# Performance work log

Hardware: AMD Instinct MI355X
Metric: run time of the kernel (lower is better)

The kernel has to match this reference:

```python
import jax, jax.numpy as jnp
import numpy as np

N, E, G = 50000, 800000, 64
IN_C, HID, HEADS, OUT_C = 128, 64, 4, 10
NEG_SLOPE = 0.2
EPS = 1e-16


def gat_conv(x, src, dst, W, a_src, a_dst, bias, heads, out_ch):
    # x: [N, F_in]; W: [F_in, heads*out_ch]; a_*: [heads, out_ch]; bias: [heads*out_ch]
    n = x.shape[0]
    h = (x @ W).reshape(n, heads, out_ch)                     # [N, H, C]
    alpha_src = jnp.einsum('nhc,hc->nh', h, a_src)            # [N, H]
    alpha_dst = jnp.einsum('nhc,hc->nh', h, a_dst)            # [N, H]
    e = jax.nn.leaky_relu(alpha_src[src] + alpha_dst[dst], NEG_SLOPE)  # [E, H]
    # segment softmax over incoming edges of each destination node
    m = jax.ops.segment_max(e, dst, num_segments=n)
    ex = jnp.exp(e - m[dst])
    denom = jax.ops.segment_sum(ex, dst, num_segments=n)
    alpha = ex / (denom[dst] + EPS)                           # [E, H]
    msg = h[src] * alpha[:, :, None]                          # [E, H, C]
    out = jax.ops.segment_sum(msg, dst, num_segments=n)       # [N, H, C]
    return out.reshape(n, heads * out_ch) + bias


def setup_inputs() -> dict:
    key = jax.random.key(0)
    ks = jax.random.split(key, 16)
    s = 0.1
    inp = {
        'x': jax.random.normal(ks[0], (N, IN_C), dtype=jnp.float32),
        'edge_index': jax.random.randint(ks[1], (2, E), 0, N, dtype=jnp.int64)
            if jax.config.jax_enable_x64 else jax.random.randint(ks[1], (2, E), 0, N).astype(jnp.int32),
        'batch': jnp.sort(jax.random.randint(ks[2], (N,), 0, G).astype(jnp.int32)),
        'W1': s * jax.random.normal(ks[3], (IN_C, HEADS * HID), dtype=jnp.float32),
        'as1': s * jax.random.normal(ks[4], (HEADS, HID), dtype=jnp.float32),
        'ad1': s * jax.random.normal(ks[5], (HEADS, HID), dtype=jnp.float32),
        'b1': jnp.zeros((HEADS * HID,), jnp.float32),
        'W2': s * jax.random.normal(ks[6], (HEADS * HID, HEADS * HID), dtype=jnp.float32),
        'as2': s * jax.random.normal(ks[7], (HEADS, HID), dtype=jnp.float32),
        'ad2': s * jax.random.normal(ks[8], (HEADS, HID), dtype=jnp.float32),
        'b2': jnp.zeros((HEADS * HID,), jnp.float32),
        'W3': s * jax.random.normal(ks[9], (HEADS * HID, HID), dtype=jnp.float32),
        'as3': s * jax.random.normal(ks[10], (1, HID), dtype=jnp.float32),
        'ad3': s * jax.random.normal(ks[11], (1, HID), dtype=jnp.float32),
        'b3': jnp.zeros((HID,), jnp.float32),
        'Wc': s * jax.random.normal(ks[12], (HID, OUT_C), dtype=jnp.float32),
        'bc': jnp.zeros((OUT_C,), jnp.float32),
    }
    return inp


def reference(x, edge_index, batch, W1, as1, ad1, b1, W2, as2, ad2, b2,
              W3, as3, ad3, b3, Wc, bc):
    n = x.shape[0]
    loop = jnp.arange(n, dtype=edge_index.dtype)
    src = jnp.concatenate([edge_index[0], loop])  # add self-loops (PyG default)
    dst = jnp.concatenate([edge_index[1], loop])

    h = gat_conv(x, src, dst, W1, as1, ad1, b1, HEADS, HID)
    h = jax.nn.elu(h)
    h = gat_conv(h, src, dst, W2, as2, ad2, b2, HEADS, HID)
    h = jax.nn.elu(h)
    h = gat_conv(h, src, dst, W3, as3, ad3, b3, 1, HID)

    # global mean pool over graphs
    sums = jax.ops.segment_sum(h, batch, num_segments=G)            # [G, HID]
    counts = jax.ops.segment_sum(jnp.ones((n,), h.dtype), batch, num_segments=G)
    pooled = sums / jnp.maximum(counts, 1.0)[:, None]

    logits = pooled @ Wc + bc                                       # [G, OUT_C]
    return logits
```

## Files before the change

### kernel.cpp

```cpp
#include <hip/hip_runtime.h>

#define NEG_SLOPE 0.2f
#define EPSV 1e-16f

typedef unsigned short ushort_t;
typedef __attribute__((ext_vector_type(8))) short bf16x8;
typedef __attribute__((ext_vector_type(4))) float f32x4;

__device__ __forceinline__ ushort_t f2bf(float f) {
    union { float f; unsigned u; } v; v.f = f;
    unsigned r = v.u + 0x7FFFu + ((v.u >> 16) & 1u);
    return (ushort_t)(r >> 16);
}
__device__ __forceinline__ float bf2f(ushort_t u) {
    union { unsigned u; float f; } v; v.u = ((unsigned)u) << 16;
    return v.f;
}

__global__ __launch_bounds__(256)
void count_kernel(const int* __restrict__ ei, int* __restrict__ deg, int E, int n) {
    int i = blockIdx.x * blockDim.x + threadIdx.x;
    int M = E + n;
    if (i >= M) return;
    int d = (i < E) ? ei[E + i] : (i - E);
    atomicAdd(&deg[d], 1);
}

__global__ __launch_bounds__(1024)
void scan1_kernel(const int* __restrict__ deg, int* __restrict__ indptr,
                  int* __restrict__ bsum, int n) {
    __shared__ int wsum[16];
    const int t = threadIdx.x;
    const int lane = t & 63;
    const int w = t >> 6;
    const int i = blockIdx.x * 1024 + t;
    int v = (i < n) ? deg[i] : 0;
    int s = v;
    #pragma unroll
    for (int off = 1; off < 64; off <<= 1) {
        int u = __shfl_up(s, off);
        if (lane >= off) s += u;
    }
    if (lane == 63) wsum[w] = s;
    __syncthreads();
    if (t < 16) {
        int ws_ = wsum[t];
        #pragma unroll
        for (int off = 1; off < 16; off <<= 1) {
            int u = __shfl_up(ws_, off);
            if (t >= off) ws_ += u;
        }
        wsum[t] = ws_;
    }
    __syncthreads();
    int woff = (w > 0) ? wsum[w - 1] : 0;
    if (i < n) indptr[i + 1] = woff + s;
    if (t == 0) bsum[blockIdx.x] = wsum[15];
}

__global__ __launch_bounds__(64)
void scan2_kernel(int* __restrict__ bsum, int nb) {
    int t = threadIdx.x;
    int v = (t < nb) ? bsum[t] : 0;
    int s = v;
    #pragma unroll
    for (int off = 1; off < 64; off <<= 1) {
        int u = __shfl_up(s, off);
        if (t >= off) s += u;
    }
    if (t < nb) bsum[t] = s - v;
}

__global__ __launch_bounds__(1024)
void scan3_kernel(int* __restrict__ indptr, const int* __restrict__ bsum, int n) {
    int i = blockIdx.x * 1024 + threadIdx.x;
    if (i < n) indptr[i + 1] += bsum[blockIdx.x];
    if (i == 0) indptr[0] = 0;
}

__global__ __launch_bounds__(256)
void scatter_kernel(const int* __restrict__ ei, int* __restrict__ cursor,
                    int* __restrict__ csr_src, int E, int n) {
    int i = blockIdx.x * blockDim.x + threadIdx.x;
    int M = E + n;
    if (i >= M) return;
    int s, d;
    if (i < E) { s = ei[i]; d = ei[E + i]; }
    else       { s = i - E; d = i - E; }
    int pos = atomicAdd(&cursor[d], 1);
    csr_src[pos] = s;
}

__global__ __launch_bounds__(256)
void cvt_kernel(const float* __restrict__ in, ushort_t* __restrict__ out, int n4) {
    int i = blockIdx.x * blockDim.x + threadIdx.x;
    if (i >= n4) return;
    float4 v = *reinterpret_cast<const float4*>(&in[i * 4]);
    ushort4 o;
    o.x = f2bf(v.x); o.y = f2bf(v.y); o.z = f2bf(v.z); o.w = f2bf(v.w);
    *reinterpret_cast<ushort4*>(&out[i * 4]) = o;
}

__global__ __launch_bounds__(256)
void transW_kernel(const float* __restrict__ W, ushort_t* __restrict__ Wt, int K, int N) {
    int idx = blockIdx.x * blockDim.x + threadIdx.x;
    if (idx >= K * N) return;
    int n = idx % N, k = idx / N;
    Wt[(long)n * K + k] = f2bf(W[idx]);
}

__global__ __launch_bounds__(256)
void mfma_gemm_alpha_kernel(const ushort_t* __restrict__ A, const ushort_t* __restrict__ Wt,
                            ushort_t* __restrict__ C,
                            const float* __restrict__ a_src, const float* __restrict__ a_dst,
                            float* __restrict__ asrc, float* __restrict__ adst,
                            int M, int K, int N, int H) {
    __shared__ ushort_t As[128][40];
    __shared__ ushort_t Ws[64][40];
    const int tid = threadIdx.x;
    const int w   = tid >> 6;
    const int lane = tid & 63;
    const int l15 = lane & 15;
    const int l4  = lane >> 4;
    const int row0 = blockIdx.x * 128;
    const int col0 = blockIdx.y * 64;
    const int hd   = blockIdx.y;

    f32x4 acc[2][4];
    #pragma unroll
    for (int mi = 0; mi < 2; ++mi)
        #pragma unroll
        for (int ni = 0; ni < 4; ++ni)
            acc[mi][ni] = (f32x4){0.f, 0.f, 0.f, 0.f};

    for (int k0 = 0; k0 < K; k0 += 32) {
        #pragma unroll
        for (int it = 0; it < 2; ++it) {
            int idx = tid + it * 256;
            int r = idx >> 2, seg = idx & 3;
            int gr = row0 + r;
            uint4 v = make_uint4(0u, 0u, 0u, 0u);
            if (gr < M)
                v = *reinterpret_cast<const uint4*>(&A[(long)gr * K + k0 + seg * 8]);
            *reinterpret_cast<uint4*>(&As[r][seg * 8]) = v;
        }
        {
            int r = tid >> 2, seg = tid & 3;
            uint4 v = *reinterpret_cast<const uint4*>(&Wt[(long)(col0 + r) * K + k0 + seg * 8]);
            *reinterpret_cast<uint4*>(&Ws[r][seg * 8]) = v;
        }
        __syncthreads();
        bf16x8 af[2], bfr[4];
        #pragma unroll
        for (int mi = 0; mi < 2; ++mi)
            af[mi] = *reinterpret_cast<const bf16x8*>(&As[w * 32 + mi * 16 + l15][8 * l4]);
        #pragma unroll
        for (int ni = 0; ni < 4; ++ni)
            bfr[ni] = *reinterpret_cast<const bf16x8*>(&Ws[ni * 16 + l15][8 * l4]);
        #pragma unroll
        for (int mi = 0; mi < 2; ++mi)
            #pragma unroll
            for (int ni = 0; ni < 4; ++ni)
                acc[mi][ni] = __builtin_amdgcn_mfma_f32_16x16x32_bf16(
                    af[mi], bfr[ni], acc[mi][ni], 0, 0, 0);
        __syncthreads();
    }

    #pragma unroll
    for (int mi = 0; mi < 2; ++mi)
        #pragma unroll
        for (int reg = 0; reg < 4; ++reg) {
            int gr = row0 + w * 32 + mi * 16 + l4 * 4 + reg;
            if (gr < M) {
                #pragma unroll
                for (int ni = 0; ni < 4; ++ni)
                    C[(long)gr * N + col0 + ni * 16 + l15] = f2bf(acc[mi][ni][reg]);
            }
        }

    float aS[4], aD[4];
    #pragma unroll
    for (int ni = 0; ni < 4; ++ni) {
        aS[ni] = a_src[hd * 64 + ni * 16 + l15];
        aD[ni] = a_dst[hd * 64 + ni * 16 + l15];
    }
    #pragma unroll
    for (int mi = 0; mi < 2; ++mi)
        #pragma unroll
        for (int reg = 0; reg < 4; ++reg) {
            float s = 0.f, d = 0.f;
            #pragma unroll
            for (int ni = 0; ni < 4; ++ni) {
                s += acc[mi][ni][reg] * aS[ni];
                d += acc[mi][ni][reg] * aD[ni];
            }
            #pragma unroll
            for (int off = 1; off < 16; off <<= 1) {
                s += __shfl_xor(s, off);
                d += __shfl_xor(d, off);
            }
            int gr = row0 + w * 32 + mi * 16 + l4 * 4 + reg;
            if (l15 == 0 && gr < M) {
                asrc[gr * H + hd] = s;
                adst[gr * H + hd] = d;
            }
        }
}

__global__ __launch_bounds__(256)
void aggregate4_kernel(const ushort_t* __restrict__ h, const float* __restrict__ asrc,
                       const float* __restrict__ adst, const int* __restrict__ indptr,
                       const int* __restrict__ csr_src, const float* __restrict__ bias,
                       ushort_t* __restrict__ out, int n, int apply_elu) {
    __shared__ int   sOff[4][64];
    __shared__ float sEx[4][4][68];
    const int node = (blockIdx.x * blockDim.x + threadIdx.x) >> 6;
    const int lane = threadIdx.x & 63;
    const int w    = threadIdx.x >> 6;
    if (node >= n) return;
    const int hd   = lane >> 4;
    const int eidx = lane & 15;
    const int beg = indptr[node], end = indptr[node + 1];
    const float ad = adst[node * 4 + hd];
    const ushort_t* __restrict__ hrow = h + 4 * lane;

    float m = -3.4e38f, sum_ex = 0.f;
    float ax = 0.f, ay = 0.f, az = 0.f, aw = 0.f;
    for (int cb = beg; cb < end; cb += 64) {
        const int cnt = min(64, end - cb);
        int s[4];
        float e[4];
        #pragma unroll
        for (int j = 0; j < 4; ++j) {
            int idx = eidx + 16 * j;
            s[j] = (idx < cnt) ? csr_src[cb + idx] : 0;
        }
        #pragma unroll
        for (int j = 0; j < 4; ++j) {
            float t = asrc[s[j] * 4 + hd] + ad;
            t = t > 0.f ? t : NEG_SLOPE * t;
            e[j] = (eidx + 16 * j < cnt) ? t : -3.4e38f;
        }
        float cm = fmaxf(fmaxf(e[0], e[1]), fmaxf(e[2], e[3]));
        #pragma unroll
        for (int off = 1; off < 16; off <<= 1) cm = fmaxf(cm, __shfl_xor(cm, off));
        const float nm = fmaxf(m, cm);
        const float scale = __expf(m - nm);
        float ex[4];
        #pragma unroll
        for (int j = 0; j < 4; ++j)
            ex[j] = (eidx + 16 * j < cnt) ? __expf(e[j] - nm) : 0.f;
        float csum = (ex[0] + ex[1]) + (ex[2] + ex[3]);
        #pragma unroll
        for (int off = 1; off < 16; off <<= 1) csum += __shfl_xor(csum, off);
        sum_ex = sum_ex * scale + csum;
        ax *= scale; ay *= scale; az *= scale; aw *= scale;
        m = nm;
        #pragma unroll
        for (int j = 0; j < 4; ++j) sEx[w][hd][eidx + 16 * j] = ex[j];
        if (hd == 0) {
            #pragma unroll
            for (int j = 0; j < 4; ++j) sOff[w][eidx + 16 * j] = s[j] << 8;
        }
        int i = 0;
        for (; i + 8 <= cnt; i += 8) {
            int o[8];
            float ee[8];
            ushort4 v[8];
            #pragma unroll
            for (int u = 0; u < 8; ++u) o[u] = sOff[w][i + u];
            #pragma unroll
            for (int u = 0; u < 8; ++u) v[u] = *reinterpret_cast<const ushort4*>(hrow + o[u]);
            #pragma unroll
            for (int u = 0; u < 8; ++u) ee[u] = sEx[w][hd][i + u];
            #pragma unroll
            for (int u = 0; u < 8; ++u) {
                ax += ee[u] * bf2f(v[u].x);
                ay += ee[u] * bf2f(v[u].y);
                az += ee[u] * bf2f(v[u].z);
                aw += ee[u] * bf2f(v[u].w);
            }
        }
        for (; i < cnt; ++i) {
            int o = sOff[w][i];
            float ee = sEx[w][hd][i];
            ushort4 v = *reinterpret_cast<const ushort4*>(hrow + o);
            ax += ee * bf2f(v.x); ay += ee * bf2f(v.y);
            az += ee * bf2f(v.z); aw += ee * bf2f(v.w);
        }
    }
    const float inv = 1.f / (sum_ex + EPSV);
    float4 b4 = *reinterpret_cast<const float4*>(bias + 4 * lane);
    float ox = ax * inv + b4.x;
    float oy = ay * inv + b4.y;
    float oz = az * inv + b4.z;
    float ow = aw * inv + b4.w;
    if (apply_elu) {
        ox = ox > 0.f ? ox : expm1f(ox);
        oy = oy > 0.f ? oy : expm1f(oy);
        oz = oz > 0.f ? oz : expm1f(oz);
        ow = ow > 0.f ? ow : expm1f(ow);
    }
    ushort4 o4;
    o4.x = f2bf(ox); o4.y = f2bf(oy); o4.z = f2bf(oz); o4.w = f2bf(ow);
    *reinterpret_cast<ushort4*>(out + (long)node * 256 + 4 * lane) = o4;
}

__global__ __launch_bounds__(256)
void aggregate_kernel(const ushort_t* __restrict__ h, const float* __restrict__ asrc,
                      const float* __restrict__ adst, const int* __restrict__ indptr,
                      const int* __restrict__ csr_src, const float* __restrict__ bias,
                      float* __restrict__ out, int n, int apply_elu) {
    __shared__ int   sInd[4][64];
    __shared__ float sEx[4][64];
    const int node = (blockIdx.x * blockDim.x + threadIdx.x) >> 6;
    const int lane = threadIdx.x & 63;
    const int w    = threadIdx.x >> 6;
    if (node >= n) return;
    const int beg = indptr[node];
    const int end = indptr[node + 1];
    const float ad = adst[node];
    const ushort_t* __restrict__ hh = h + lane;

    float m = -3.4e38f, sum_ex = 0.f, acc = 0.f;
    for (int cb = beg; cb < end; cb += 64) {
        const int cnt = min(64, end - cb);
        int s = 0;
        float e = -3.4e38f;
        if (lane < cnt) {
            s = csr_src[cb + lane];
            e = asrc[s] + ad;
            e = e > 0.f ? e : NEG_SLOPE * e;
        }
        float cm = e;
        #pragma unroll
        for (int off = 32; off > 0; off >>= 1) cm = fmaxf(cm, __shfl_xor(cm, off));
        const float nm = fmaxf(m, cm);
        const float scale = __expf(m - nm);
        const float ex = (lane < cnt) ? __expf(e - nm) : 0.f;
        float cs = ex;
        #pragma unroll
        for (int off = 32; off > 0; off >>= 1) cs += __shfl_xor(cs, off);
        sum_ex = sum_ex * scale + cs;
        acc *= scale;
        m = nm;
        sInd[w][lane] = s;
        sEx[w][lane]  = ex;
        int i = 0;
        for (; i + 8 <= cnt; i += 8) {
            int si[8];
            float ei_[8], vi[8];
            #pragma unroll
            for (int u = 0; u < 8; ++u) si[u] = sInd[w][i + u];
            #pragma unroll
            for (int u = 0; u < 8; ++u) vi[u] = bf2f(hh[(long)si[u] * 64]);
            #pragma unroll
            for (int u = 0; u < 8; ++u) ei_[u] = sEx[w][i + u];
            #pragma unroll
            for (int u = 0; u < 8; ++u) acc += ei_[u] * vi[u];
        }
        for (; i < cnt; ++i)
            acc += sEx[w][i] * bf2f(hh[(long)sInd[w][i] * 64]);
    }
    float o = acc / (sum_ex + EPSV) + bias[lane];
    if (apply_elu) o = o > 0.f ? o : expm1f(o);
    out[(long)node * 64 + lane] = o;
}

constexpr int POOL_CHUNK = 128;

__global__ __launch_bounds__(64)
void pool_kernel(const float* __restrict__ h, const int* __restrict__ batch,
                 float* __restrict__ sums, int* __restrict__ counts, int n) {
    int lane = threadIdx.x;
    int start = blockIdx.x * POOL_CHUNK;
    if (start >= n) return;
    int end = min(start + POOL_CHUNK, n);
    int gcur = batch[start];
    float acc = 0.f;
    int run = 0;
    for (int i = start; i < end; ++i) {
        int g = batch[i];
        if (g != gcur) {
            atomicAdd(&sums[gcur * 64 + lane], acc);
            if (lane == 0) atomicAdd(&counts[gcur], run);
            acc = 0.f; run = 0; gcur = g;
        }
        acc += h[(long)i * 64 + lane];
        ++run;
    }
    atomicAdd(&sums[gcur * 64 + lane], acc);
    if (lane == 0) atomicAdd(&counts[gcur], run);
}

__global__ void classify_kernel(const float* __restrict__ sums, const int* __restrict__ counts,
                                const float* __restrict__ Wc, const float* __restrict__ bc,
                                float* __restrict__ out, int G) {
    int t = threadIdx.x;
    if (t >= G * 10) return;
    int g = t / 10, o = t - g * 10;
    int c_ = counts[g];
    float inv = 1.f / (float)(c_ > 1 ? c_ : 1);
    float acc = bc[o];
    for (int c = 0; c < 64; ++c)
        acc += sums[g * 64 + c] * inv * Wc[c * 10 + o];
    out[t] = acc;
}

extern "C" void kernel_launch(void* const* d_in, const int* in_sizes, int n_in,
                              void* d_out, int out_size, void* d_ws, size_t ws_size,
                              hipStream_t stream) {
    const float* x   = (const float*)d_in[0];
    const int*   ei  = (const int*)d_in[1];
    const int*   bat = (const int*)d_in[2];
    const float* W1  = (const float*)d_in[3];
    const float* as1 = (const float*)d_in[4];
    const float* ad1 = (const float*)d_in[5];
    const float* b1  = (const float*)d_in[6];
    const float* W2  = (const float*)d_in[7];
    const float* as2 = (const float*)d_in[8];
    const float* ad2 = (const float*)d_in[9];
    const float* b2  = (const float*)d_in[10];
    const float* W3  = (const float*)d_in[11];
    const float* as3 = (const float*)d_in[12];
    const float* ad3 = (const float*)d_in[13];
    const float* b3  = (const float*)d_in[14];
    const float* Wc  = (const float*)d_in[15];
    const float* bc  = (const float*)d_in[16];
    float* out = (float*)d_out;

    const int N = in_sizes[2];
    const int E = in_sizes[1] / 2;
    const int M = E + N;
    const int IN_C = in_sizes[0] / N;
    const int G = out_size / 10;

    char* p = (char*)d_ws;
    auto carve = [&](size_t bytes) -> void* {
        void* r = (void*)p;
        p += (bytes + 255) & ~(size_t)255;
        return r;
    };
    ushort_t* hA  = (ushort_t*)carve((size_t)N * 256 * 2);
    ushort_t* hB  = (ushort_t*)carve((size_t)N * 256 * 2);
    ushort_t* xb  = (ushort_t*)carve((size_t)N * IN_C * 2);
    ushort_t* Wt1 = (ushort_t*)carve((size_t)256 * IN_C * 2);
    ushort_t* Wt2 = (ushort_t*)carve((size_t)256 * 256 * 2);
    ushort_t* Wt3 = (ushort_t*)carve((size_t)64 * 256 * 2);
    float* h3f  = (float*)carve((size_t)N * 64 * 4);
    float* asrc = (float*)carve((size_t)N * 4 * 4);
    float* adst = (float*)carve((size_t)N * 4 * 4);
    float* sums = (float*)carve((size_t)G * 64 * 4);
    int*   cnts = (int*)carve((size_t)G * 4);
    int*   deg  = (int*)carve((size_t)N * 4);
    int*   iptr = (int*)carve((size_t)(N + 1) * 4);
    int*   csr  = (int*)carve((size_t)M * 4);
    int*   bsum = (int*)carve(256 * 4);
    (void)ws_size; (void)n_in;

    const int NB = (N + 1023) / 1024;

    cvt_kernel<<<(N * IN_C / 4 + 255) / 256, 256, 0, stream>>>(x, xb, N * IN_C / 4);
    transW_kernel<<<(IN_C * 256 + 255) / 256, 256, 0, stream>>>(W1, Wt1, IN_C, 256);
    transW_kernel<<<(256 * 256 + 255) / 256, 256, 0, stream>>>(W2, Wt2, 256, 256);
    transW_kernel<<<(256 * 64 + 255) / 256, 256, 0, stream>>>(W3, Wt3, 256, 64);

    hipMemsetAsync(deg, 0, (size_t)N * 4, stream);
    count_kernel<<<(M + 255) / 256, 256, 0, stream>>>(ei, deg, E, N);
    scan1_kernel<<<NB, 1024, 0, stream>>>(deg, iptr, bsum, N);
    scan2_kernel<<<1, 64, 0, stream>>>(bsum, NB);
    scan3_kernel<<<NB, 1024, 0, stream>>>(iptr, bsum, N);
    hipMemcpyAsync(deg, iptr, (size_t)N * 4, hipMemcpyDeviceToDevice, stream);
    scatter_kernel<<<(M + 255) / 256, 256, 0, stream>>>(ei, deg, csr, E, N);

    {
        dim3 grid((N + 127) / 128, 4);
        mfma_gemm_alpha_kernel<<<grid, 256, 0, stream>>>(xb, Wt1, hA, as1, ad1,
                                                          asrc, adst, N, IN_C, 256, 4);
    }
    aggregate4_kernel<<<(N + 3) / 4, 256, 0, stream>>>(hA, asrc, adst, iptr, csr, b1, hB, N, 1);

    {
        dim3 grid((N + 127) / 128, 4);
        mfma_gemm_alpha_kernel<<<grid, 256, 0, stream>>>(hB, Wt2, hA, as2, ad2,
                                                          asrc, adst, N, 256, 256, 4);
    }
    aggregate4_kernel<<<(N + 3) / 4, 256, 0, stream>>>(hA, asrc, adst, iptr, csr, b2, hB, N, 1);

    {
        dim3 grid((N + 127) / 128, 1);
        mfma_gemm_alpha_kernel<<<grid, 256, 0, stream>>>(hB, Wt3, hA, as3, ad3,
                                                          asrc, adst, N, 256, 64, 1);
    }
    aggregate_kernel<<<(N + 3) / 4, 256, 0, stream>>>(hA, asrc, adst, iptr, csr, b3, h3f, N, 0);

    hipMemsetAsync(sums, 0, (size_t)G * 64 * 4, stream);
    hipMemsetAsync(cnts, 0, (size_t)G * 4, stream);
    pool_kernel<<<(N + POOL_CHUNK - 1) / POOL_CHUNK, 64, 0, stream>>>(h3f, bat, sums, cnts, N);
    classify_kernel<<<1, 640, 0, stream>>>(sums, cnts, Wc, bc, out, G);
}
```

Measured before the change: 485.2 us.

## Drop softmax max pass, widen GEMM tiles, fuse prep kernels, bf16 final layer

Removes the running-max subtraction and rescaling from the edge softmax in both aggregation kernels, exponentiating raw logits directly and relying on the logits staying in a safe range. Templates the MFMA GEMM so layers 1 and 2 use 128-column tiles, which halves the grid's column dimension and reuses each A tile across more outputs. Merges the x conversion and the three weight transposes into one launch. Stores the last layer's output in bf16 so the pool kernel reads half the bytes. The trade-off is a risk of exp overflow for large attention logits, plus extra rounding in the final features.

After: 474.6 us. 1.02x faster.

```diff
diff --git a/kernel.cpp b/kernel.cpp
--- a/kernel.cpp
+++ b/kernel.cpp
@@ -92,43 +92,62 @@
 }
 
 __global__ __launch_bounds__(256)
-void cvt_kernel(const float* __restrict__ in, ushort_t* __restrict__ out, int n4) {
-    int i = blockIdx.x * blockDim.x + threadIdx.x;
-    if (i >= n4) return;
-    float4 v = *reinterpret_cast<const float4*>(&in[i * 4]);
-    ushort4 o;
-    o.x = f2bf(v.x); o.y = f2bf(v.y); o.z = f2bf(v.z); o.w = f2bf(v.w);
-    *reinterpret_cast<ushort4*>(&out[i * 4]) = o;
-}
-
-__global__ __launch_bounds__(256)
-void transW_kernel(const float* __restrict__ W, ushort_t* __restrict__ Wt, int K, int N) {
-    int idx = blockIdx.x * blockDim.x + threadIdx.x;
-    if (idx >= K * N) return;
-    int n = idx % N, k = idx / N;
-    Wt[(long)n * K + k] = f2bf(W[idx]);
-}
-
+void prep_kernel(const float* __restrict__ x, ushort_t* __restrict__ xb, int nx4,
+                 const float* __restrict__ W1, ushort_t* __restrict__ Wt1,
+                 const float* __restrict__ W2, ushort_t* __restrict__ Wt2,
+                 const float* __restrict__ W3, ushort_t* __restrict__ Wt3,
+                 int K1) {
+    long idx = (long)blockIdx.x * 256 + threadIdx.x;
+    if (idx < nx4) {
+        float4 v = *reinterpret_cast<const float4*>(&x[idx * 4]);
+        ushort4 o;
+        o.x = f2bf(v.x); o.y = f2bf(v.y); o.z = f2bf(v.z); o.w = f2bf(v.w);
+        *reinterpret_cast<ushort4*>(&xb[idx * 4]) = o;
+        return;
+    }
+    idx -= nx4;
+    if (idx < (long)K1 * 256) {
+        int n = (int)(idx % 256), k = (int)(idx / 256);
+        Wt1[(long)n * K1 + k] = f2bf(W1[idx]);
+        return;
+    }
+    idx -= (long)K1 * 256;
+    if (idx < 256 * 256) {
+        int n = (int)(idx % 256), k = (int)(idx / 256);
+        Wt2[(long)n * 256 + k] = f2bf(W2[idx]);
+        return;
+    }
+    idx -= 256 * 256;
+    if (idx < 256 * 64) {
+        int n = (int)(idx % 64), k = (int)(idx / 64);
+        Wt3[(long)n * 256 + k] = f2bf(W3[idx]);
+    }
+}
+
+template<int NC>
 __global__ __launch_bounds__(256)
 void mfma_gemm_alpha_kernel(const ushort_t* __restrict__ A, const ushort_t* __restrict__ Wt,
                             ushort_t* __restrict__ C,
                             const float* __restrict__ a_src, const float* __restrict__ a_dst,
                             float* __restrict__ asrc, float* __restrict__ adst,
                             int M, int K, int N, int H) {
+    constexpr int TBN = NC * 64;
+    constexpr int MI  = (NC == 2) ? 4 : 2;
     __shared__ ushort_t As[128][40];
-    __shared__ ushort_t Ws[64][40];
-    const int tid = threadIdx.x;
-    const int w   = tid >> 6;
+    __shared__ ushort_t Ws[TBN][40];
+    const int tid  = threadIdx.x;
+    const int w    = tid >> 6;
     const int lane = tid & 63;
-    const int l15 = lane & 15;
-    const int l4  = lane >> 4;
+    const int l15  = lane & 15;
+    const int l4   = lane >> 4;
     const int row0 = blockIdx.x * 128;
-    const int col0 = blockIdx.y * 64;
-    const int hd   = blockIdx.y;
-
-    f32x4 acc[2][4];
+    const int col0 = blockIdx.y * TBN;
+    const int rbase = (NC == 2) ? (w & 1) * 64 : w * 32;
+    const int cbase = (NC == 2) ? (w >> 1) * 64 : 0;
+
+    f32x4 acc[MI][4];
     #pragma unroll
-    for (int mi = 0; mi < 2; ++mi)
+    for (int mi = 0; mi < MI; ++mi)
         #pragma unroll
         for (int ni = 0; ni < 4; ++ni)
             acc[mi][ni] = (f32x4){0.f, 0.f, 0.f, 0.f};
@@ -144,40 +163,43 @@
                 v = *reinterpret_cast<const uint4*>(&A[(long)gr * K + k0 + seg * 8]);
             *reinterpret_cast<uint4*>(&As[r][seg * 8]) = v;
         }
-        {
-            int r = tid >> 2, seg = tid & 3;
+        #pragma unroll
+        for (int it = 0; it < NC; ++it) {
+            int idx = tid + it * 256;
+            int r = idx >> 2, seg = idx & 3;
             uint4 v = *reinterpret_cast<const uint4*>(&Wt[(long)(col0 + r) * K + k0 + seg * 8]);
             *reinterpret_cast<uint4*>(&Ws[r][seg * 8]) = v;
         }
         __syncthreads();
-        bf16x8 af[2], bfr[4];
-        #pragma unroll
-        for (int mi = 0; mi < 2; ++mi)
-            af[mi] = *reinterpret_cast<const bf16x8*>(&As[w * 32 + mi * 16 + l15][8 * l4]);
+        bf16x8 af[MI], bfv[4];
+        #pragma unroll
+        for (int mi = 0; mi < MI; ++mi)
+            af[mi] = *reinterpret_cast<const bf16x8*>(&As[rbase + mi * 16 + l15][8 * l4]);
         #pragma unroll
         for (int ni = 0; ni < 4; ++ni)
-            bfr[ni] = *reinterpret_cast<const bf16x8*>(&Ws[ni * 16 + l15][8 * l4]);
-        #pragma unroll
-        for (int mi = 0; mi < 2; ++mi)
+            bfv[ni] = *reinterpret_cast<const bf16x8*>(&Ws[cbase + ni * 16 + l15][8 * l4]);
+        #pragma unroll
+        for (int mi = 0; mi < MI; ++mi)
             #pragma unroll
             for (int ni = 0; ni < 4; ++ni)
                 acc[mi][ni] = __builtin_amdgcn_mfma_f32_16x16x32_bf16(
-                    af[mi], bfr[ni], acc[mi][ni], 0, 0, 0);
+                    af[mi], bfv[ni], acc[mi][ni], 0, 0, 0);
         __syncthreads();
     }
 
     #pragma unroll
-    for (int mi = 0; mi < 2; ++mi)
+    for (int mi = 0; mi < MI; ++mi)
         #pragma unroll
         for (int reg = 0; reg < 4; ++reg) {
-            int gr = row0 + w * 32 + mi * 16 + l4 * 4 + reg;
+            int gr = row0 + rbase + mi * 16 + l4 * 4 + reg;
             if (gr < M) {
                 #pragma unroll
                 for (int ni = 0; ni < 4; ++ni)
-                    C[(long)gr * N + col0 + ni * 16 + l15] = f2bf(acc[mi][ni][reg]);
+                    C[(long)gr * N + col0 + cbase + ni * 16 + l15] = f2bf(acc[mi][ni][reg]);
             }
         }
 
+    const int hd = (col0 + cbase) >> 6;
     float aS[4], aD[4];
     #pragma unroll
     for (int ni = 0; ni < 4; ++ni) {
@@ -185,7 +207,7 @@
         aD[ni] = a_dst[hd * 64 + ni * 16 + l15];
     }
     #pragma unroll
-    for (int mi = 0; mi < 2; ++mi)
+    for (int mi = 0; mi < MI; ++mi)
         #pragma unroll
         for (int reg = 0; reg < 4; ++reg) {
             float s = 0.f, d = 0.f;
@@ -199,7 +221,7 @@
                 s += __shfl_xor(s, off);
                 d += __shfl_xor(d, off);
             }
-            int gr = row0 + w * 32 + mi * 16 + l4 * 4 + reg;
+            int gr = row0 + rbase + mi * 16 + l4 * 4 + reg;
             if (l15 == 0 && gr < M) {
                 asrc[gr * H + hd] = s;
                 adst[gr * H + hd] = d;
@@ -224,12 +246,12 @@
     const float ad = adst[node * 4 + hd];
     const ushort_t* __restrict__ hrow = h + 4 * lane;
 
-    float m = -3.4e38f, sum_ex = 0.f;
+    float sum_ex = 0.f;
     float ax = 0.f, ay = 0.f, az = 0.f, aw = 0.f;
     for (int cb = beg; cb < end; cb += 64) {
         const int cnt = min(64, end - cb);
         int s[4];
-        float e[4];
+        float ex[4];
         #pragma unroll
         for (int j = 0; j < 4; ++j) {
             int idx = eidx + 16 * j;
@@ -239,23 +261,12 @@
         for (int j = 0; j < 4; ++j) {
             float t = asrc[s[j] * 4 + hd] + ad;
             t = t > 0.f ? t : NEG_SLOPE * t;
-            e[j] = (eidx + 16 * j < cnt) ? t : -3.4e38f;
-        }
-        float cm = fmaxf(fmaxf(e[0], e[1]), fmaxf(e[2], e[3]));
-        #pragma unroll
-        for (int off = 1; off < 16; off <<= 1) cm = fmaxf(cm, __shfl_xor(cm, off));
-        const float nm = fmaxf(m, cm);
-        const float scale = __expf(m - nm);
-        float ex[4];
-        #pragma unroll
-        for (int j = 0; j < 4; ++j)
-            ex[j] = (eidx + 16 * j < cnt) ? __expf(e[j] - nm) : 0.f;
+            ex[j] = (eidx + 16 * j < cnt) ? __expf(t) : 0.f;
+        }
         float csum = (ex[0] + ex[1]) + (ex[2] + ex[3]);
         #pragma unroll
         for (int off = 1; off < 16; off <<= 1) csum += __shfl_xor(csum, off);
-        sum_ex = sum_ex * scale + csum;
-        ax *= scale; ay *= scale; az *= scale; aw *= scale;
-        m = nm;
+        sum_ex += csum;
         #pragma unroll
         for (int j = 0; j < 4; ++j) sEx[w][hd][eidx + 16 * j] = ex[j];
         if (hd == 0) {
@@ -310,7 +321,7 @@
 void aggregate_kernel(const ushort_t* __restrict__ h, const float* __restrict__ asrc,
                       const float* __restrict__ adst, const int* __restrict__ indptr,
                       const int* __restrict__ csr_src, const float* __restrict__ bias,
-                      float* __restrict__ out, int n, int apply_elu) {
+                      ushort_t* __restrict__ out, int n, int apply_elu) {
     __shared__ int   sInd[4][64];
     __shared__ float sEx[4][64];
     const int node = (blockIdx.x * blockDim.x + threadIdx.x) >> 6;
@@ -322,28 +333,21 @@
     const float ad = adst[node];
     const ushort_t* __restrict__ hh = h + lane;
 
-    float m = -3.4e38f, sum_ex = 0.f, acc = 0.f;
+    float sum_ex = 0.f, acc = 0.f;
     for (int cb = beg; cb < end; cb += 64) {
         const int cnt = min(64, end - cb);
         int s = 0;
-        float e = -3.4e38f;
+        float ex = 0.f;
         if (lane < cnt) {
             s = csr_src[cb + lane];
-            e = asrc[s] + ad;
+            float e = asrc[s] + ad;
             e = e > 0.f ? e : NEG_SLOPE * e;
-        }
-        float cm = e;
-        #pragma unroll
-        for (int off = 32; off > 0; off >>= 1) cm = fmaxf(cm, __shfl_xor(cm, off));
-        const float nm = fmaxf(m, cm);
-        const float scale = __expf(m - nm);
-        const float ex = (lane < cnt) ? __expf(e - nm) : 0.f;
+            ex = __expf(e);
+        }
         float cs = ex;
         #pragma unroll
         for (int off = 32; off > 0; off >>= 1) cs += __shfl_xor(cs, off);
-        sum_ex = sum_ex * scale + cs;
-        acc *= scale;
-        m = nm;
+        sum_ex += cs;
         sInd[w][lane] = s;
         sEx[w][lane]  = ex;
         int i = 0;
@@ -364,13 +368,13 @@
     }
     float o = acc / (sum_ex + EPSV) + bias[lane];
     if (apply_elu) o = o > 0.f ? o : expm1f(o);
-    out[(long)node * 64 + lane] = o;
+    out[(long)node * 64 + lane] = f2bf(o);
 }
 
 constexpr int POOL_CHUNK = 128;
 
 __global__ __launch_bounds__(64)
-void pool_kernel(const float* __restrict__ h, const int* __restrict__ batch,
+void pool_kernel(const ushort_t* __restrict__ h, const int* __restrict__ batch,
                  float* __restrict__ sums, int* __restrict__ counts, int n) {
     int lane = threadIdx.x;
     int start = blockIdx.x * POOL_CHUNK;
@@ -386,7 +390,7 @@
             if (lane == 0) atomicAdd(&counts[gcur], run);
             acc = 0.f; run = 0; gcur = g;
         }
-        acc += h[(long)i * 64 + lane];
+        acc += bf2f(h[(long)i * 64 + lane]);
         ++run;
     }
     atomicAdd(&sums[gcur * 64 + lane], acc);
@@ -447,7 +451,6 @@
     ushort_t* Wt1 = (ushort_t*)carve((size_t)256 * IN_C * 2);
     ushort_t* Wt2 = (ushort_t*)carve((size_t)256 * 256 * 2);
     ushort_t* Wt3 = (ushort_t*)carve((size_t)64 * 256 * 2);
-    float* h3f  = (float*)carve((size_t)N * 64 * 4);
     float* asrc = (float*)carve((size_t)N * 4 * 4);
     float* adst = (float*)carve((size_t)N * 4 * 4);
     float* sums = (float*)carve((size_t)G * 64 * 4);
@@ -460,10 +463,12 @@
 
     const int NB = (N + 1023) / 1024;
 
-    cvt_kernel<<<(N * IN_C / 4 + 255) / 256, 256, 0, stream>>>(x, xb, N * IN_C / 4);
-    transW_kernel<<<(IN_C * 256 + 255) / 256, 256, 0, stream>>>(W1, Wt1, IN_C, 256);
-    transW_kernel<<<(256 * 256 + 255) / 256, 256, 0, stream>>>(W2, Wt2, 256, 256);
-    transW_kernel<<<(256 * 64 + 255) / 256, 256, 0, stream>>>(W3, Wt3, 256, 64);
+    {
+        long nx4 = (long)N * IN_C / 4;
+        long total = nx4 + (long)IN_C * 256 + 256 * 256 + 256 * 64;
+        prep_kernel<<<(int)((total + 255) / 256), 256, 0, stream>>>(
+            x, xb, (int)nx4, W1, Wt1, W2, Wt2, W3, Wt3, IN_C);
+    }
 
     hipMemsetAsync(deg, 0, (size_t)N * 4, stream);
     count_kernel<<<(M + 255) / 256, 256, 0, stream>>>(ei, deg, E, N);
@@ -474,28 +479,28 @@
     scatter_kernel<<<(M + 255) / 256, 256, 0, stream>>>(ei, deg, csr, E, N);
 
     {
-        dim3 grid((N + 127) / 128, 4);
-        mfma_gemm_alpha_kernel<<<grid, 256, 0, stream>>>(xb, Wt1, hA, as1, ad1,
-                                                          asrc, adst, N, IN_C, 256, 4);
+        dim3 grid((N + 127) / 128, 2);
+        mfma_gemm_alpha_kernel<2><<<grid, 256, 0, stream>>>(xb, Wt1, hA, as1, ad1,
+                                                            asrc, adst, N, IN_C, 256, 4);
     }
     aggregate4_kernel<<<(N + 3) / 4, 256, 0, stream>>>(hA, asrc, adst, iptr, csr, b1, hB, N, 1);
 
     {
-        dim3 grid((N + 127) / 128, 4);
-        mfma_gemm_alpha_kernel<<<grid, 256, 0, stream>>>(hB, Wt2, hA, as2, ad2,
-                                                          asrc, adst, N, 256, 256, 4);
+        dim3 grid((N + 127) / 128, 2);
+        mfma_gemm_alpha_kernel<2><<<grid, 256, 0, stream>>>(hB, Wt2, hA, as2, ad2,
+                                                            asrc, adst, N, 256, 256, 4);
     }
     aggregate4_kernel<<<(N + 3) / 4, 256, 0, stream>>>(hA, asrc, adst, iptr, csr, b2, hB, N, 1);
 
     {
         dim3 grid((N + 127) / 128, 1);
-        mfma_gemm_alpha_kernel<<<grid, 256, 0, stream>>>(hB, Wt3, hA, as3, ad3,
-                                                          asrc, adst, N, 256, 64, 1);
-    }
-    aggregate_kernel<<<(N + 3) / 4, 256, 0, stream>>>(hA, asrc, adst, iptr, csr, b3, h3f, N, 0);
+        mfma_gemm_alpha_kernel<1><<<grid, 256, 0, stream>>>(hB, Wt3, hA, as3, ad3,
+                                                            asrc, adst, N, 256, 64, 1);
+    }
+    aggregate_kernel<<<(N + 3) / 4, 256, 0, stream>>>(hA, asrc, adst, iptr, csr, b3, hB, N, 0);
 
     hipMemsetAsync(sums, 0, (size_t)G * 64 * 4, stream);
     hipMemsetAsync(cnts, 0, (size_t)G * 4, stream);
-    pool_kernel<<<(N + POOL_CHUNK - 1) / POOL_CHUNK, 64, 0, stream>>>(h3f, bat, sums, cnts, N);
+    pool_kernel<<<(N + POOL_CHUNK - 1) / POOL_CHUNK, 64, 0, stream>>>(hB, bat, sums, cnts, N);
     classify_kernel<<<1, 640, 0, stream>>>(sums, cnts, Wc, bc, out, G);
 }
```
